# Optimization experiments

Measured on AMD Instinct MI355X. Metric: run time of the kernel, lower is better.

## Reference

```python
import jax, jax.numpy as jnp
import numpy as np

B = 256          # number of queries
N = 200_000      # active nodes (hidden rows / scatter dim)
E = 400_000      # edges
D = 128          # in_dim == out_dim
ATTN = 128       # attn_dim
N_REL = 24
REL_VOCAB = 2 * N_REL + 3   # 2*n_rel + 1 + 2
N_NODE = 100_000


def setup_inputs() -> dict:
    key = jax.random.key(0)
    ks = jax.random.split(key, 16)
    # forward args
    q_sub = jax.random.randint(ks[0], (B,), 0, N_NODE)
    q_rel = jax.random.randint(ks[1], (B,), 0, REL_VOCAB)
    hidden = jax.random.normal(ks[2], (N, D), dtype=jnp.float32) * 0.05
    # edges columns: [query_idx, unused, rel, tail_entity, sub_local, obj_local]
    e_q = jax.random.randint(ks[3], (E,), 0, B)
    e_unused = jnp.zeros((E,), dtype=jnp.int64)
    e_rel = jax.random.randint(ks[4], (E,), 0, REL_VOCAB)
    e_tail = jax.random.randint(ks[5], (E,), 0, N_NODE)
    e_sub = jax.random.randint(ks[6], (E,), 0, N)
    e_obj = jax.random.randint(ks[7], (E,), 0, N)
    edges = jnp.stack([e_q, e_unused, e_rel, e_tail, e_sub, e_obj], axis=1)
    nodes = jnp.stack([jax.random.randint(ks[8], (N,), 0, B),
                       jax.random.randint(ks[9], (N,), 0, N_NODE)], axis=1)
    # parameters
    rela_embed = jax.random.normal(ks[10], (REL_VOCAB, D), dtype=jnp.float32) * 0.05
    Ws = jax.random.normal(ks[11], (D, ATTN), dtype=jnp.float32) * 0.05
    Wr = jax.random.normal(ks[12], (D, ATTN), dtype=jnp.float32) * 0.05
    Wqr_w = jax.random.normal(ks[13], (D, ATTN), dtype=jnp.float32) * 0.05
    Wqr_b = jnp.zeros((ATTN,), dtype=jnp.float32)
    walpha_w = jax.random.normal(ks[14], (ATTN, 1), dtype=jnp.float32) * 0.05
    walpha_b = jnp.zeros((1,), dtype=jnp.float32)
    Wh = jax.random.normal(ks[15], (D, D), dtype=jnp.float32) * 0.05
    return {"q_sub": q_sub, "q_rel": q_rel, "hidden": hidden, "edges": edges,
            "nodes": nodes, "rela_embed": rela_embed, "Ws": Ws, "Wr": Wr,
            "Wqr_w": Wqr_w, "Wqr_b": Wqr_b, "walpha_w": walpha_w,
            "walpha_b": walpha_b, "Wh": Wh}


def reference(q_sub, q_rel, hidden, edges, nodes, rela_embed, Ws, Wr,
              Wqr_w, Wqr_b, walpha_w, walpha_b, Wh):
    # id_layer == 0 < n_layer-1: no edge filtering branch, act = identity
    sampled_nodes_idx = (nodes[:, 1] > -1) & (nodes[:, 1] < N_NODE + 1)
    sub = edges[:, 4]
    rel = edges[:, 2]
    obj = edges[:, 5]
    r_idx = edges[:, 0]
    hs = hidden[sub]                      # [E, D] gather
    hr = rela_embed[rel]                  # [E, D] gather
    h_qr = rela_embed[q_rel][r_idx]       # [B, D] -> [E, D] gather
    # fused attention MLP: sigmoid(w_alpha(relu(Ws hs + Wr hr + Wqr h_qr + b)))
    pre = jax.nn.relu(hs @ Ws + hr @ Wr + h_qr @ Wqr_w + Wqr_b)   # [E, ATTN]
    alpha = jax.nn.sigmoid(pre @ walpha_w + walpha_b)             # [E, 1]
    message = alpha * (hs + hr)                                   # [E, D]
    message_agg = jax.ops.segment_sum(message, obj, num_segments=N)  # [N, D]
    hidden_new = message_agg @ Wh                                 # [N, D]
    return hidden_new, alpha, sampled_nodes_idx
```

## Files before the change

### kernel.cpp

```cpp
#include <hip/hip_runtime.h>
#include <hip/hip_bf16.h>
#include <math.h>

#define DIM 128
#define N_NODE_C 100000

typedef __attribute__((ext_vector_type(8))) short  bf16x8;
typedef __attribute__((ext_vector_type(4))) float  f32x4;

__device__ inline unsigned short f2bf_rne(float f) {
    unsigned u = __float_as_uint(f);
    return (unsigned short)((u + 0x7FFFu + ((u >> 16) & 1u)) >> 16);
}
__device__ inline float bf2f(unsigned short u) {
    return __uint_as_float(((unsigned)u) << 16);
}

__global__ __launch_bounds__(128) void setup_kernel(
    const int* __restrict__ q_rel,
    const float* __restrict__ rela,
    const float* __restrict__ Wqr_w,
    const float* __restrict__ Wqr_b,
    const float* __restrict__ Wr,
    const float* __restrict__ Ws,
    const float* __restrict__ Wh,
    float* __restrict__ qrW,
    float* __restrict__ relhr,
    uint4* __restrict__ wpack_s,
    uint4* __restrict__ wpack_h,
    int* deg, int N,
    int B, int RV)
{
    const int blk = blockIdx.x;
    const int j   = threadIdx.x;

    if (blk < B + RV) {
        __shared__ float emb[DIM];
        const float* W;
        float* out;
        float bias = 0.f;
        int row;
        if (blk < B) {
            row  = q_rel[blk];
            W    = Wqr_w;
            out  = qrW + (size_t)blk * DIM;
            bias = Wqr_b[j];
        } else {
            row = blk - B;
            W   = Wr;
            out = relhr + (size_t)(blk - B) * 256;
        }
        emb[j] = rela[(size_t)row * DIM + j];
        __syncthreads();

        float acc = bias;
#pragma unroll 8
        for (int k = 0; k < DIM; ++k)
            acc += emb[k] * W[k * DIM + j];
        out[j] = acc;
        if (blk >= B)
            out[128 + j] = emb[j];
        return;
    }

    if (blk < B + RV + 32) {
        const int pid = blk - (B + RV);
        const float* W = (pid < 16) ? Ws : Wh;
        uint4* dst     = (pid < 16) ? wpack_s : wpack_h;
        const int id   = (pid & 15) * 128 + j;
        const int ct   = id >> 8;
        const int kb   = (id >> 6) & 3;
        const int lane = id & 63;
        const int col  = ct * 16 + (lane & 15);
        const int k0   = kb * 32 + (lane >> 4) * 8;

        unsigned v[4];
#pragma unroll
        for (int p = 0; p < 4; ++p) {
            unsigned lo = f2bf_rne(W[(size_t)(k0 + 2 * p)     * DIM + col]);
            unsigned hi = f2bf_rne(W[(size_t)(k0 + 2 * p + 1) * DIM + col]);
            v[p] = lo | (hi << 16);
        }
        dst[id] = make_uint4(v[0], v[1], v[2], v[3]);
        return;
    }

    if (deg) {
        int i = (blk - (B + RV + 32)) * 128 + j;
        if (i < N) deg[i] = 0;
    }
}

__global__ __launch_bounds__(256) void gemm_hist_kernel(
    const float* __restrict__ A, const uint4* __restrict__ Wpack,
    unsigned short* __restrict__ H, int M,
    const int* __restrict__ edges, int* __restrict__ deg, int E, int Nb)
{
    if ((int)blockIdx.x >= Nb) {
        int i = ((int)blockIdx.x - Nb) * 256 + threadIdx.x;
        if (i < E) atomicAdd(&deg[edges[(size_t)i * 6 + 5]], 1);
        return;
    }

    __shared__ uint4 wlds[2048];
    const int t = threadIdx.x;
#pragma unroll
    for (int p = 0; p < 8; ++p)
        wlds[p * 256 + t] = Wpack[p * 256 + t];
    __syncthreads();

    const int wave = t >> 6;
    const int lane = t & 63;
    const int r    = lane & 15;
    const int g    = lane >> 4;
    const int row0 = blockIdx.x * 64 + wave * 16;

    int arow = row0 + r;
    if (arow >= M) arow = M - 1;
    const float* Ap = A + (size_t)arow * DIM + g * 8;

    bf16x8 afrag[4];
#pragma unroll
    for (int kb = 0; kb < 4; ++kb) {
        const float4 lo = *(const float4*)(Ap + kb * 32);
        const float4 hi = *(const float4*)(Ap + kb * 32 + 4);
        bf16x8 a;
        a[0] = (short)f2bf_rne(lo.x); a[1] = (short)f2bf_rne(lo.y);
        a[2] = (short)f2bf_rne(lo.z); a[3] = (short)f2bf_rne(lo.w);
        a[4] = (short)f2bf_rne(hi.x); a[5] = (short)f2bf_rne(hi.y);
        a[6] = (short)f2bf_rne(hi.z); a[7] = (short)f2bf_rne(hi.w);
        afrag[kb] = a;
    }

#pragma unroll
    for (int kb = 0; kb < 4; ++kb)
        *(bf16x8*)&H[(size_t)arow * 256 + kb * 32 + g * 8] = afrag[kb];

#pragma unroll
    for (int ct = 0; ct < 8; ++ct) {
        f32x4 acc = {0.f, 0.f, 0.f, 0.f};
#pragma unroll
        for (int kb = 0; kb < 4; ++kb) {
            bf16x8 b = *(bf16x8*)&wlds[ct * 256 + kb * 64 + lane];
            acc = __builtin_amdgcn_mfma_f32_16x16x32_bf16(afrag[kb], b, acc, 0, 0, 0);
        }
        const int col = ct * 16 + r;
#pragma unroll
        for (int jj = 0; jj < 4; ++jj) {
            const int row = row0 + g * 4 + jj;
            if (row < M)
                H[(size_t)row * 256 + 128 + col] = f2bf_rne(acc[jj]);
        }
    }
}

__global__ __launch_bounds__(256) void gemm_mfma_f32(
    const float* A, const uint4* __restrict__ Wpack, float* C, int M)
{
    __shared__ uint4 wlds[2048];
    const int t = threadIdx.x;
#pragma unroll
    for (int p = 0; p < 8; ++p)
        wlds[p * 256 + t] = Wpack[p * 256 + t];
    __syncthreads();

    const int wave = t >> 6;
    const int lane = t & 63;
    const int r    = lane & 15;
    const int g    = lane >> 4;
    const int row0 = blockIdx.x * 64 + wave * 16;

    int arow = row0 + r;
    if (arow >= M) arow = M - 1;
    const float* Ap = A + (size_t)arow * DIM + g * 8;

    bf16x8 afrag[4];
#pragma unroll
    for (int kb = 0; kb < 4; ++kb) {
        const float4 lo = *(const float4*)(Ap + kb * 32);
        const float4 hi = *(const float4*)(Ap + kb * 32 + 4);
        bf16x8 a;
        a[0] = (short)f2bf_rne(lo.x); a[1] = (short)f2bf_rne(lo.y);
        a[2] = (short)f2bf_rne(lo.z); a[3] = (short)f2bf_rne(lo.w);
        a[4] = (short)f2bf_rne(hi.x); a[5] = (short)f2bf_rne(hi.y);
        a[6] = (short)f2bf_rne(hi.z); a[7] = (short)f2bf_rne(hi.w);
        afrag[kb] = a;
    }

#pragma unroll
    for (int ct = 0; ct < 8; ++ct) {
        f32x4 acc = {0.f, 0.f, 0.f, 0.f};
#pragma unroll
        for (int kb = 0; kb < 4; ++kb) {
            bf16x8 b = *(bf16x8*)&wlds[ct * 256 + kb * 64 + lane];
            acc = __builtin_amdgcn_mfma_f32_16x16x32_bf16(afrag[kb], b, acc, 0, 0, 0);
        }
        const int col = ct * 16 + r;
#pragma unroll
        for (int jj = 0; jj < 4; ++jj) {
            const int row = row0 + g * 4 + jj;
            if (row < M)
                C[(size_t)row * DIM + col] = acc[jj];
        }
    }
}

__global__ __launch_bounds__(256) void scan1_kernel(
    const int* __restrict__ in, int* __restrict__ out,
    int* __restrict__ bsum, int n)
{
    __shared__ int ts[256];
    const int tid  = threadIdx.x;
    const int base = blockIdx.x * 2048 + tid * 8;

    int v[8];
    int run = 0;
#pragma unroll
    for (int i = 0; i < 8; ++i) {
        int x = (base + i < n) ? in[base + i] : 0;
        v[i] = run;
        run += x;
    }
    ts[tid] = run;
    __syncthreads();
    for (int off = 1; off < 256; off <<= 1) {
        int x = (tid >= off) ? ts[tid - off] : 0;
        __syncthreads();
        ts[tid] += x;
        __syncthreads();
    }
    const int excl = ts[tid] - run;
#pragma unroll
    for (int i = 0; i < 8; ++i)
        if (base + i < n) out[base + i] = v[i] + excl;
    if (tid == 255) bsum[blockIdx.x] = ts[255];
}

__global__ __launch_bounds__(256) void scan3_kernel(
    int* __restrict__ offs, int* __restrict__ cursor,
    const int* __restrict__ bsum,
    const int* __restrict__ nodes, float* __restrict__ samp, int n)
{
    __shared__ int pref;
    if (threadIdx.x == 0) {
        int run = 0;
        const int lim = blockIdx.x >> 3;
        for (int i = 0; i < lim; ++i) run += bsum[i];
        pref = run;
    }
    __syncthreads();
    int i = blockIdx.x * 256 + threadIdx.x;
    if (i < n) {
        int v = offs[i] + pref;
        offs[i]   = v;
        cursor[i] = v;
        int nv = nodes[(size_t)i * 2 + 1];
        samp[i] = (nv > -1 && nv < N_NODE_C + 1) ? 1.f : 0.f;
    }
}

__global__ __launch_bounds__(256) void scatter_kernel(
    const int* __restrict__ edges, int* __restrict__ cursor,
    int4* __restrict__ esorted, int E)
{
    int i = blockIdx.x * 256 + threadIdx.x;
    if (i < E) {
        int4 rec;
        rec.x = edges[(size_t)i * 6 + 0];
        rec.y = edges[(size_t)i * 6 + 2];
        rec.z = edges[(size_t)i * 6 + 4];
        rec.w = i;
        int obj = edges[(size_t)i * 6 + 5];
        int pos = atomicAdd(&cursor[obj], 1);
        esorted[pos] = rec;
    }
}

__device__ inline void edge_compute(
    const int4 rec, const bf16x8 hb, const bf16x8 pb,
    const float* __restrict__ relhr, const float* __restrict__ qrW,
    const float4 wwA, const float4 wwB, const float wb,
    int j, int l16,
    float4& accA, float4& accB, float* __restrict__ alpha_out)
{
    const float* rr = &relhr[(size_t)rec.y * 256];
    const float4 bA  = *(const float4*)&rr[j];
    const float4 bB  = *(const float4*)&rr[j + 4];
    const float4 rvA = *(const float4*)&rr[128 + j];
    const float4 rvB = *(const float4*)&rr[128 + j + 4];
    const float4 cA  = *(const float4*)&qrW[(size_t)rec.x * DIM + j];
    const float4 cB  = *(const float4*)&qrW[(size_t)rec.x * DIM + j + 4];

    float sdot =
        fmaxf(bf2f((unsigned short)pb[0]) + bA.x + cA.x, 0.f) * wwA.x +
        fmaxf(bf2f((unsigned short)pb[1]) + bA.y + cA.y, 0.f) * wwA.y +
        fmaxf(bf2f((unsigned short)pb[2]) + bA.z + cA.z, 0.f) * wwA.z +
        fmaxf(bf2f((unsigned short)pb[3]) + bA.w + cA.w, 0.f) * wwA.w +
        fmaxf(bf2f((unsigned short)pb[4]) + bB.x + cB.x, 0.f) * wwB.x +
        fmaxf(bf2f((unsigned short)pb[5]) + bB.y + cB.y, 0.f) * wwB.y +
        fmaxf(bf2f((unsigned short)pb[6]) + bB.z + cB.z, 0.f) * wwB.z +
        fmaxf(bf2f((unsigned short)pb[7]) + bB.w + cB.w, 0.f) * wwB.w;

#pragma unroll
    for (int off = 8; off >= 1; off >>= 1)
        sdot += __shfl_xor(sdot, off, 16);

    const float alpha =
        __builtin_amdgcn_rcpf(1.f + __expf(-(sdot + wb)));

    accA.x += alpha * (bf2f((unsigned short)hb[0]) + rvA.x);
    accA.y += alpha * (bf2f((unsigned short)hb[1]) + rvA.y);
    accA.z += alpha * (bf2f((unsigned short)hb[2]) + rvA.z);
    accA.w += alpha * (bf2f((unsigned short)hb[3]) + rvA.w);
    accB.x += alpha * (bf2f((unsigned short)hb[4]) + rvB.x);
    accB.y += alpha * (bf2f((unsigned short)hb[5]) + rvB.y);
    accB.z += alpha * (bf2f((unsigned short)hb[6]) + rvB.z);
    accB.w += alpha * (bf2f((unsigned short)hb[7]) + rvB.w);

    if (l16 == 0) alpha_out[rec.w] = alpha;
}

__global__ __launch_bounds__(256) void node_agg_kernel(
    const int4* __restrict__ esorted,
    const unsigned short* __restrict__ hsub,
    const float* __restrict__ relhr,
    const float* __restrict__ qrW,
    const float* __restrict__ walpha_w,
    const float* __restrict__ walpha_b,
    const int* __restrict__ deg,
    const int* __restrict__ offs,
    float* __restrict__ agg,
    float* __restrict__ alpha_out,
    int N)
{
    const int o = (blockIdx.x * 256 + threadIdx.x) >> 4;
    if (o >= N) return;
    const int l16 = threadIdx.x & 15;
    const int j   = l16 * 8;

    const int d = deg[o];
    const int s = offs[o];

    const float4 wwA = *(const float4*)&walpha_w[j];
    const float4 wwB = *(const float4*)&walpha_w[j + 4];
    const float  wb  = walpha_b[0];

    float4 accA = make_float4(0.f, 0.f, 0.f, 0.f);
    float4 accB = make_float4(0.f, 0.f, 0.f, 0.f);

    if (d > 0) {
        if (d <= 4) {
            int4 rec[4];
#pragma unroll
            for (int k = 0; k < 4; ++k)
                if (k < d) rec[k] = esorted[s + k];
            bf16x8 hb[4], pb[4];
#pragma unroll
            for (int k = 0; k < 4; ++k)
                if (k < d) {
                    hb[k] = *(const bf16x8*)&hsub[(size_t)rec[k].z * 256 + j];
                    pb[k] = *(const bf16x8*)&hsub[(size_t)rec[k].z * 256 + 128 + j];
                }
#pragma unroll
            for (int k = 0; k < 4; ++k)
                if (k < d)
                    edge_compute(rec[k], hb[k], pb[k], relhr, qrW,
                                 wwA, wwB, wb, j, l16, accA, accB, alpha_out);
        } else {
            int4 rec = esorted[s];
            for (int k = 0; k < d; ++k) {
                const int4 nrec = (k + 1 < d) ? esorted[s + k + 1] : rec;
                const bf16x8 hb = *(const bf16x8*)&hsub[(size_t)rec.z * 256 + j];
                const bf16x8 pb = *(const bf16x8*)&hsub[(size_t)rec.z * 256 + 128 + j];
                edge_compute(rec, hb, pb, relhr, qrW,
                             wwA, wwB, wb, j, l16, accA, accB, alpha_out);
                rec = nrec;
            }
        }
    }

    *(float4*)&agg[(size_t)o * DIM + j]     = accA;
    *(float4*)&agg[(size_t)o * DIM + j + 4] = accB;
}

__global__ __launch_bounds__(256) void edge_kernel_fb(
    const int* __restrict__ edges,
    const float* __restrict__ hidden,
    const float* __restrict__ rela,
    const float* __restrict__ Ws,
    const float* __restrict__ qrW,
    const float* __restrict__ relhr,
    const float* __restrict__ walpha_w,
    const float* __restrict__ walpha_b,
    float* __restrict__ agg,
    float* __restrict__ alpha_out,
    int E)
{
    const int widx = threadIdx.x >> 6;
    const int lane = threadIdx.x & 63;
    const int e    = blockIdx.x * 4 + widx;
    const bool valid = (e < E);
    const int ec   = valid ? e : 0;

    const int r_idx = edges[(size_t)ec * 6 + 0];
    const int rel   = edges[(size_t)ec * 6 + 2];
    const int sub   = edges[(size_t)ec * 6 + 4];
    const int obj   = edges[(size_t)ec * 6 + 5];

    const int j = lane * 2;

    const float2 hv = *(const float2*)&hidden[(size_t)sub * DIM + j];
    const float2 rv = *(const float2*)&rela[(size_t)rel * DIM + j];

    __shared__ float hrow[4][DIM];
    *(float2*)&hrow[widx][j] = hv;
    __syncthreads();
    float p0 = 0.f, p1 = 0.f;
#pragma unroll 4
    for (int k = 0; k < DIM; ++k) {
        float hk  = hrow[widx][k];
        float2 w2 = *(const float2*)&Ws[k * DIM + j];
        p0 += hk * w2.x;
        p1 += hk * w2.y;
    }

    const float2 b2 = *(const float2*)&relhr[(size_t)rel * 256 + j];
    const float2 c2 = *(const float2*)&qrW[(size_t)r_idx * DIM + j];
    p0 = fmaxf(p0 + b2.x + c2.x, 0.f);
    p1 = fmaxf(p1 + b2.y + c2.y, 0.f);

    const float2 ww = *(const float2*)&walpha_w[j];
    float s = p0 * ww.x + p1 * ww.y;
#pragma unroll
    for (int off = 32; off >= 1; off >>= 1)
        s += __shfl_xor(s, off, 64);

    const float alpha = 1.f / (1.f + expf(-(s + walpha_b[0])));

    if (valid) {
        const float m0 = alpha * (hv.x + rv.x);
        const float m1 = alpha * (hv.y + rv.y);
        atomicAdd(&agg[(size_t)obj * DIM + j], m0);
        atomicAdd(&agg[(size_t)obj * DIM + j + 1], m1);
        if (lane == 0) alpha_out[e] = alpha;
    }
}

__global__ __launch_bounds__(256, 3) void gemm_n128(
    const float* A,
    const float* __restrict__ W,
    float* C,
    int M)
{
    __shared__ __align__(16) float Alds[64][DIM];
    __shared__ __align__(16) float Wlds[32][DIM];

    const int t    = threadIdx.x;
    const int row0 = blockIdx.x * 64;
    const int tx   = t & 31;
    const int ty   = t >> 5;

#pragma unroll
    for (int p = 0; p < 8; ++p) {
        int idx = p * 1024 + t * 4;
        int r   = idx >> 7;
        int c   = idx & 127;
        int gr  = row0 + r;
        if (gr >= M) gr = M - 1;
        *(float4*)&Alds[r][c] = *(const float4*)&A[(size_t)gr * DIM + c];
    }

    float acc[8][4] = {};

    for (int kk = 0; kk < 4; ++kk) {
        __syncthreads();
        {
            const float* Wg = W + (size_t)kk * 32 * DIM;
#pragma unroll
            for (int p = 0; p < 4; ++p) {
                int idx = p * 1024 + t * 4;
                *(float4*)&Wlds[idx >> 7][idx & 127] = *(const float4*)&Wg[idx];
            }
        }
        __syncthreads();

#pragma unroll 2
        for (int k4 = 0; k4 < 32; k4 += 4) {
            const float4 w0 = *(const float4*)&Wlds[k4 + 0][tx * 4];
            const float4 w1 = *(const float4*)&Wlds[k4 + 1][tx * 4];
            const float4 w2 = *(const float4*)&Wlds[k4 + 2][tx * 4];
            const float4 w3 = *(const float4*)&Wlds[k4 + 3][tx * 4];
#pragma unroll
            for (int i = 0; i < 8; ++i) {
                const float4 a = *(const float4*)&Alds[ty * 8 + i][kk * 32 + k4];
                acc[i][0] = fmaf(a.w, w3.x, fmaf(a.z, w2.x, fmaf(a.y, w1.x, fmaf(a.x, w0.x, acc[i][0]))));
                acc[i][1] = fmaf(a.w, w3.y, fmaf(a.z, w2.y, fmaf(a.y, w1.y, fmaf(a.x, w0.y, acc[i][1]))));
                acc[i][2] = fmaf(a.w, w3.z, fmaf(a.z, w2.z, fmaf(a.y, w1.z, fmaf(a.x, w0.z, acc[i][2]))));
                acc[i][3] = fmaf(a.w, w3.w, fmaf(a.z, w2.w, fmaf(a.y, w1.w, fmaf(a.x, w0.w, acc[i][3]))));
            }
        }
    }
    __syncthreads();

#pragma unroll
    for (int i = 0; i < 8; ++i) {
        int gr = row0 + ty * 8 + i;
        if (gr < M) {
            float4 v = make_float4(acc[i][0], acc[i][1], acc[i][2], acc[i][3]);
            *(float4*)&C[(size_t)gr * DIM + tx * 4] = v;
        }
    }
}

__global__ __launch_bounds__(256) void nodes_kernel(
    const int* __restrict__ nodes, float* __restrict__ out, int N)
{
    int i = blockIdx.x * 256 + threadIdx.x;
    if (i < N) {
        int v = nodes[(size_t)i * 2 + 1];
        out[i] = (v > -1 && v < N_NODE_C + 1) ? 1.f : 0.f;
    }
}

extern "C" void kernel_launch(void* const* d_in, const int* in_sizes, int n_in,
                              void* d_out, int out_size, void* d_ws, size_t ws_size,
                              hipStream_t stream)
{
    const int*   q_rel    = (const int*)d_in[1];
    const float* hidden   = (const float*)d_in[2];
    const int*   edges    = (const int*)d_in[3];
    const int*   nodes    = (const int*)d_in[4];
    const float* rela     = (const float*)d_in[5];
    const float* Ws       = (const float*)d_in[6];
    const float* Wr       = (const float*)d_in[7];
    const float* Wqr_w    = (const float*)d_in[8];
    const float* Wqr_b    = (const float*)d_in[9];
    const float* walpha_w = (const float*)d_in[10];
    const float* walpha_b = (const float*)d_in[11];
    const float* Wh       = (const float*)d_in[12];

    const int B  = in_sizes[1];
    const int N  = in_sizes[2] / DIM;
    const int E  = in_sizes[3] / 6;
    const int RV = in_sizes[5] / DIM;

    float* out       = (float*)d_out;
    float* agg       = out;
    float* alpha_out = out + (size_t)N * DIM;
    float* samp      = alpha_out + (size_t)E;

    char* p = (char*)d_ws;
    float* qrW   = (float*)p;     p += (size_t)B * DIM * sizeof(float);
    float* relhr = (float*)p;     p += (size_t)RV * 256 * sizeof(float);
    uint4* wpack_s = (uint4*)p;   p += 2048 * sizeof(uint4);
    uint4* wpack_h = (uint4*)p;   p += 2048 * sizeof(uint4);
    int4*  esorted = (int4*)p;    p += (size_t)E * sizeof(int4);
    unsigned short* hsub = (unsigned short*)p;
    p += (size_t)N * 256 * sizeof(unsigned short);
    const size_t pre_int_bytes = (size_t)(p - (char*)d_ws);
    const size_t need_A = pre_int_bytes + ((size_t)3 * N + 128) * sizeof(int);

    const bool tierA = (ws_size >= need_A);

    int* deg = nullptr;
    int* offs = nullptr;
    int* cursor = nullptr;
    int* bsum = nullptr;
    if (tierA) {
        char* q = (char*)d_ws + pre_int_bytes;
        deg    = (int*)q;
        offs   = deg + N;
        cursor = offs + N;
        bsum   = cursor + N;
    }

    const int ZB = tierA ? (N + 127) / 128 : 0;
    setup_kernel<<<B + RV + 32 + ZB, 128, 0, stream>>>(
        q_rel, rela, Wqr_w, Wqr_b, Wr, Ws, Wh,
        qrW, relhr, wpack_s, wpack_h, deg, N, B, RV);

    if (tierA) {
        const int Nb = (N + 63) / 64;
        const int Hb = (E + 255) / 256;
        gemm_hist_kernel<<<Nb + Hb, 256, 0, stream>>>(
            hidden, wpack_s, hsub, N, edges, deg, E, Nb);

        const int nb = (N + 2047) / 2048;
        scan1_kernel<<<nb, 256, 0, stream>>>(deg, offs, bsum, N);
        scan3_kernel<<<(N + 255) / 256, 256, 0, stream>>>(
            offs, cursor, bsum, nodes, samp, N);
        scatter_kernel<<<(E + 255) / 256, 256, 0, stream>>>(
            edges, cursor, esorted, E);

        node_agg_kernel<<<(N * 16 + 255) / 256, 256, 0, stream>>>(
            esorted, hsub, relhr, qrW, walpha_w, walpha_b,
            deg, offs, agg, alpha_out, N);

        gemm_mfma_f32<<<(N + 63) / 64, 256, 0, stream>>>(agg, wpack_h, out, N);
    } else {
        hipMemsetAsync(agg, 0, (size_t)N * DIM * sizeof(float), stream);
        edge_kernel_fb<<<(E + 3) / 4, 256, 0, stream>>>(
            edges, hidden, rela, Ws, qrW, relhr, walpha_w, walpha_b,
            agg, alpha_out, E);
        gemm_n128<<<(N + 63) / 64, 256, 0, stream>>>(agg, Wh, out, N);
        nodes_kernel<<<(N + 255) / 256, 256, 0, stream>>>(nodes, samp, N);
    }
}
```

Measured before the change: 234.4 us.

## Fuse node aggregation with the Wh projection GEMM in one kernel

The per-node aggregation kernel now stages each block's 16 aggregated rows as bf16 in shared memory and multiplies them by Wh with MFMA before writing the output. This removes the separate GEMM launch and the full fp32 round trip of the N×128 aggregate through global memory. The small-degree unrolled path with prefetched edges is dropped in favour of the single pipelined loop. In exchange every block of 16 nodes reloads the 32 KB packed Wh into LDS, which raises per-block overhead and LDS use and may lower occupancy.

Result: faster. 210.4 us (-10.2%).

```diff
diff --git a/kernel.cpp b/kernel.cpp
--- a/kernel.cpp
+++ b/kernel.cpp
@@ -154,57 +154,6 @@
     }
 }
 
-__global__ __launch_bounds__(256) void gemm_mfma_f32(
-    const float* A, const uint4* __restrict__ Wpack, float* C, int M)
-{
-    __shared__ uint4 wlds[2048];
-    const int t = threadIdx.x;
-#pragma unroll
-    for (int p = 0; p < 8; ++p)
-        wlds[p * 256 + t] = Wpack[p * 256 + t];
-    __syncthreads();
-
-    const int wave = t >> 6;
-    const int lane = t & 63;
-    const int r    = lane & 15;
-    const int g    = lane >> 4;
-    const int row0 = blockIdx.x * 64 + wave * 16;
-
-    int arow = row0 + r;
-    if (arow >= M) arow = M - 1;
-    const float* Ap = A + (size_t)arow * DIM + g * 8;
-
-    bf16x8 afrag[4];
-#pragma unroll
-    for (int kb = 0; kb < 4; ++kb) {
-        const float4 lo = *(const float4*)(Ap + kb * 32);
-        const float4 hi = *(const float4*)(Ap + kb * 32 + 4);
-        bf16x8 a;
-        a[0] = (short)f2bf_rne(lo.x); a[1] = (short)f2bf_rne(lo.y);
-        a[2] = (short)f2bf_rne(lo.z); a[3] = (short)f2bf_rne(lo.w);
-        a[4] = (short)f2bf_rne(hi.x); a[5] = (short)f2bf_rne(hi.y);
-        a[6] = (short)f2bf_rne(hi.z); a[7] = (short)f2bf_rne(hi.w);
-        afrag[kb] = a;
-    }
-
-#pragma unroll
-    for (int ct = 0; ct < 8; ++ct) {
-        f32x4 acc = {0.f, 0.f, 0.f, 0.f};
-#pragma unroll
-        for (int kb = 0; kb < 4; ++kb) {
-            bf16x8 b = *(bf16x8*)&wlds[ct * 256 + kb * 64 + lane];
-            acc = __builtin_amdgcn_mfma_f32_16x16x32_bf16(afrag[kb], b, acc, 0, 0, 0);
-        }
-        const int col = ct * 16 + r;
-#pragma unroll
-        for (int jj = 0; jj < 4; ++jj) {
-            const int row = row0 + g * 4 + jj;
-            if (row < M)
-                C[(size_t)row * DIM + col] = acc[jj];
-        }
-    }
-}
-
 __global__ __launch_bounds__(256) void scan1_kernel(
     const int* __restrict__ in, int* __restrict__ out,
     int* __restrict__ bsum, int n)
@@ -320,7 +269,7 @@
     if (l16 == 0) alpha_out[rec.w] = alpha;
 }
 
-__global__ __launch_bounds__(256) void node_agg_kernel(
+__global__ __launch_bounds__(256) void node_agg_fused(
     const int4* __restrict__ esorted,
     const unsigned short* __restrict__ hsub,
     const float* __restrict__ relhr,
@@ -329,44 +278,35 @@
     const float* __restrict__ walpha_b,
     const int* __restrict__ deg,
     const int* __restrict__ offs,
-    float* __restrict__ agg,
+    const uint4* __restrict__ wpack_h,
+    float* __restrict__ outC,
     float* __restrict__ alpha_out,
     int N)
 {
-    const int o = (blockIdx.x * 256 + threadIdx.x) >> 4;
-    if (o >= N) return;
-    const int l16 = threadIdx.x & 15;
+    __shared__ unsigned short tile[16][136];
+    __shared__ uint4 wlds[2048];
+
+    const int t = threadIdx.x;
+#pragma unroll
+    for (int p = 0; p < 8; ++p)
+        wlds[p * 256 + t] = wpack_h[p * 256 + t];
+
+    const int g16 = t >> 4;
+    const int l16 = t & 15;
     const int j   = l16 * 8;
-
-    const int d = deg[o];
-    const int s = offs[o];
-
-    const float4 wwA = *(const float4*)&walpha_w[j];
-    const float4 wwB = *(const float4*)&walpha_w[j + 4];
-    const float  wb  = walpha_b[0];
+    const int o   = blockIdx.x * 16 + g16;
 
     float4 accA = make_float4(0.f, 0.f, 0.f, 0.f);
     float4 accB = make_float4(0.f, 0.f, 0.f, 0.f);
 
-    if (d > 0) {
-        if (d <= 4) {
-            int4 rec[4];
-#pragma unroll
-            for (int k = 0; k < 4; ++k)
-                if (k < d) rec[k] = esorted[s + k];
-            bf16x8 hb[4], pb[4];
-#pragma unroll
-            for (int k = 0; k < 4; ++k)
-                if (k < d) {
-                    hb[k] = *(const bf16x8*)&hsub[(size_t)rec[k].z * 256 + j];
-                    pb[k] = *(const bf16x8*)&hsub[(size_t)rec[k].z * 256 + 128 + j];
-                }
-#pragma unroll
-            for (int k = 0; k < 4; ++k)
-                if (k < d)
-                    edge_compute(rec[k], hb[k], pb[k], relhr, qrW,
-                                 wwA, wwB, wb, j, l16, accA, accB, alpha_out);
-        } else {
+    if (o < N) {
+        const int d = deg[o];
+        const int s = offs[o];
+        if (d > 0) {
+            const float4 wwA = *(const float4*)&walpha_w[j];
+            const float4 wwB = *(const float4*)&walpha_w[j + 4];
+            const float  wb  = walpha_b[0];
+
             int4 rec = esorted[s];
             for (int k = 0; k < d; ++k) {
                 const int4 nrec = (k + 1 < d) ? esorted[s + k + 1] : rec;
@@ -379,8 +319,43 @@
         }
     }
 
-    *(float4*)&agg[(size_t)o * DIM + j]     = accA;
-    *(float4*)&agg[(size_t)o * DIM + j + 4] = accB;
+    {
+        bf16x8 ob;
+        ob[0] = (short)f2bf_rne(accA.x); ob[1] = (short)f2bf_rne(accA.y);
+        ob[2] = (short)f2bf_rne(accA.z); ob[3] = (short)f2bf_rne(accA.w);
+        ob[4] = (short)f2bf_rne(accB.x); ob[5] = (short)f2bf_rne(accB.y);
+        ob[6] = (short)f2bf_rne(accB.z); ob[7] = (short)f2bf_rne(accB.w);
+        *(bf16x8*)&tile[g16][j] = ob;
+    }
+    __syncthreads();
+
+    const int wave = t >> 6;
+    const int lane = t & 63;
+    const int r    = lane & 15;
+    const int g    = lane >> 4;
+
+    bf16x8 afrag[4];
+#pragma unroll
+    for (int kb = 0; kb < 4; ++kb)
+        afrag[kb] = *(const bf16x8*)&tile[r][kb * 32 + g * 8];
+
+#pragma unroll
+    for (int cti = 0; cti < 2; ++cti) {
+        const int ct = wave * 2 + cti;
+        f32x4 acc = {0.f, 0.f, 0.f, 0.f};
+#pragma unroll
+        for (int kb = 0; kb < 4; ++kb) {
+            bf16x8 b = *(bf16x8*)&wlds[ct * 256 + kb * 64 + lane];
+            acc = __builtin_amdgcn_mfma_f32_16x16x32_bf16(afrag[kb], b, acc, 0, 0, 0);
+        }
+        const int col = ct * 16 + r;
+#pragma unroll
+        for (int jj = 0; jj < 4; ++jj) {
+            const int row = blockIdx.x * 16 + g * 4 + jj;
+            if (row < N)
+                outC[(size_t)row * DIM + col] = acc[jj];
+        }
+    }
 }
 
 __global__ __launch_bounds__(256) void edge_kernel_fb(
@@ -545,7 +520,7 @@
     const int RV = in_sizes[5] / DIM;
 
     float* out       = (float*)d_out;
-    float* agg       = out;
+    float* hidnew    = out;
     float* alpha_out = out + (size_t)N * DIM;
     float* samp      = alpha_out + (size_t)E;
 
@@ -592,17 +567,15 @@
         scatter_kernel<<<(E + 255) / 256, 256, 0, stream>>>(
             edges, cursor, esorted, E);
 
-        node_agg_kernel<<<(N * 16 + 255) / 256, 256, 0, stream>>>(
+        node_agg_fused<<<(N + 15) / 16, 256, 0, stream>>>(
             esorted, hsub, relhr, qrW, walpha_w, walpha_b,
-            deg, offs, agg, alpha_out, N);
-
-        gemm_mfma_f32<<<(N + 63) / 64, 256, 0, stream>>>(agg, wpack_h, out, N);
+            deg, offs, wpack_h, hidnew, alpha_out, N);
     } else {
-        hipMemsetAsync(agg, 0, (size_t)N * DIM * sizeof(float), stream);
+        hipMemsetAsync(hidnew, 0, (size_t)N * DIM * sizeof(float), stream);
         edge_kernel_fb<<<(E + 3) / 4, 256, 0, stream>>>(
             edges, hidden, rela, Ws, qrW, relhr, walpha_w, walpha_b,
-            agg, alpha_out, E);
-        gemm_n128<<<(N + 63) / 64, 256, 0, stream>>>(agg, Wh, out, N);
+            hidnew, alpha_out, E);
+        gemm_n128<<<(N + 63) / 64, 256, 0, stream>>>(hidnew, Wh, hidnew, N);
         nodes_kernel<<<(N + 255) / 256, 256, 0, stream>>>(nodes, samp, N);
     }
 }
```
